# Performance work log

Measured on AMD Instinct MI355X. Metric: run time of the kernel, lower is better.

The kernel has to match this reference:

```python
import jax, jax.numpy as jnp
import numpy as np

N_ITEMS = 1_000_000
IN_DIM, HID_DIM, OUT_DIM = 64, 256, 128
N_BINS = 4096


def setup_inputs() -> dict:
    key = jax.random.key(0)
    k1, k2, k3, k4 = jax.random.split(key, 4)
    x = jax.random.normal(k1, (N_ITEMS, IN_DIM), dtype=jnp.float32)
    idxs = jax.random.randint(k2, (N_ITEMS,), 0, N_BINS, dtype=jnp.int64)
    W1 = jax.random.normal(k3, (IN_DIM, HID_DIM), dtype=jnp.float32) * (1.0 / np.sqrt(IN_DIM))
    b1 = jnp.zeros((HID_DIM,), dtype=jnp.float32)
    W2 = jax.random.normal(k4, (HID_DIM, OUT_DIM), dtype=jnp.float32) * (1.0 / np.sqrt(HID_DIM))
    b2 = jnp.zeros((OUT_DIM,), dtype=jnp.float32)
    return {"x": x, "idxs": idxs, "n_bins": N_BINS, "W1": W1, "b1": b1, "W2": W2, "b2": b2}


def reference(x, idxs, n_bins, W1, b1, W2, b2):
    # MLP: Linear -> ReLU -> Linear (per item)
    h = jax.nn.relu(x @ W1 + b1)            # [N, HID]
    items_encoded = h @ W2 + b2             # [N, OUT]
    # scatter-add into bins (torch.index_put_ with accumulate=True)
    embeddings = jax.ops.segment_sum(items_encoded, idxs, num_segments=n_bins)  # [n_bins, OUT]
    return embeddings
```

## Files before the change

### kernel.cpp

```cpp
#include <hip/hip_runtime.h>
#include <hip/hip_bf16.h>

typedef __attribute__((ext_vector_type(8))) short short8;
typedef __attribute__((ext_vector_type(4))) float f32x4;
typedef __attribute__((ext_vector_type(4))) int int4v;

#define CAPB  384
#define NSCAT 64
#define NBINS 4096

__device__ inline unsigned short f2bf(float f) {
  unsigned u = __float_as_uint(f);
  return (unsigned short)((u + 0x7FFFu + ((u >> 16) & 1u)) >> 16);
}
__device__ inline short bfc(float f) {
  __hip_bfloat16 h = __float2bfloat16(f);
  return *(short*)&h;
}
__device__ inline __attribute__((always_inline))
f32x4 mfma16(short8 a, short8 b, f32x4 c) {
  return __builtin_amdgcn_mfma_f32_16x16x32_bf16(a, b, c, 0, 0, 0);
}
__device__ __forceinline__ void gload_lds16(const void* g, void* l) {
  __builtin_amdgcn_global_load_lds(
      (const __attribute__((address_space(1))) void*)g,
      (__attribute__((address_space(3))) void*)l, 16, 0, 0);
}

__global__ __launch_bounds__(256)
void bin_hist(const int* __restrict__ idxs, int* __restrict__ wsCnt,
              int* __restrict__ wsOff, int n_items)
{
  __shared__ int hist[NBINS];
  const int tid = threadIdx.x;
  for (int b = tid; b < NBINS; b += 256) hist[b] = 0;
  __syncthreads();

  const int nq = n_items >> 2;
  const int chunk = (nq + NSCAT - 1) / NSCAT;
  const int s0 = blockIdx.x * chunk;
  const int s1 = min(nq, s0 + chunk);
  const int4v* idx4 = (const int4v*)idxs;
  for (int s = s0 + tid; s < s1; s += 256) {
    int4v v = idx4[s];
    atomicAdd(&hist[v[0]], 1);
    atomicAdd(&hist[v[1]], 1);
    atomicAdd(&hist[v[2]], 1);
    atomicAdd(&hist[v[3]], 1);
  }
  if (blockIdx.x == NSCAT - 1)
    for (int i = (nq << 2) + tid; i < n_items; i += 256)
      atomicAdd(&hist[idxs[i]], 1);
  __syncthreads();

  for (int b = tid; b < NBINS; b += 256) {
    int c = hist[b];
    if (c) wsOff[b * NSCAT + blockIdx.x] = atomicAdd(&wsCnt[b], c);
  }
}

__global__ __launch_bounds__(256)
void scatter_ids(const int* __restrict__ idxs, const int* __restrict__ wsOff,
                 int* __restrict__ wsIds, int n_items)
{
  __shared__ int cur[NBINS];
  const int tid = threadIdx.x;
  for (int b = tid; b < NBINS; b += 256) cur[b] = wsOff[b * NSCAT + blockIdx.x];
  __syncthreads();

  const int nq = n_items >> 2;
  const int chunk = (nq + NSCAT - 1) / NSCAT;
  const int s0 = blockIdx.x * chunk;
  const int s1 = min(nq, s0 + chunk);
  const int4v* idx4 = (const int4v*)idxs;
  for (int s = s0 + tid; s < s1; s += 256) {
    int4v v = idx4[s];
    #pragma unroll
    for (int e = 0; e < 4; ++e) {
      int b = v[e];
      int pos = atomicAdd(&cur[b], 1);
      if (pos < CAPB) wsIds[b * CAPB + pos] = s * 4 + e;
    }
  }
  if (blockIdx.x == NSCAT - 1)
    for (int i = (nq << 2) + tid; i < n_items; i += 256) {
      int b = idxs[i];
      int pos = atomicAdd(&cur[b], 1);
      if (pos < CAPB) wsIds[b * CAPB + pos] = i;
    }
}

#define LDS_BYTES 153344

__global__ __launch_bounds__(512)
void mlp_bin8(const float* __restrict__ x,
              const float* __restrict__ W1,
              const float* __restrict__ b1,
              const float* __restrict__ W2,
              const float* __restrict__ b2,
              const int* __restrict__ wsCnt,
              const int* __restrict__ wsIds,
              float* __restrict__ out)
{
  extern __shared__ char smem[];
  unsigned short* sW1 = (unsigned short*)smem;
  char*           sStage = smem + 32768;
  unsigned short* sW2 = (unsigned short*)(smem + 32768);
  float* sB1 = (float*)(smem + 131072);
  float* sB2 = (float*)(smem + 132096);
  unsigned short* sHs = (unsigned short*)(smem + 132608);
  int*   sIds = (int*)(smem + 141056);

  const int tid = threadIdx.x;
  const int myblk = blockIdx.x;

  for (int f = tid; f < 16384; f += 512) {
    int blk = f >> 9;
    int mt = blk >> 1, kt = blk & 1;
    int ln = (f >> 3) & 63, j = f & 7;
    int qq = ln >> 4, cc = ln & 15;
    sW1[f] = f2bf(W1[(32*kt + 8*qq + j)*256 + 16*mt + cc]);
  }
  if (tid < 256) sB1[tid] = b1[tid];
  if (tid < 128) sB2[tid] = b2[tid];
  __syncthreads();

  const int lane = tid & 63;
  const int wave = tid >> 6;
  const int c = lane & 15;
  const int q = lane >> 4;
  char* myStage = sStage + wave * 12288;
  int*  myIds   = sIds + wave * 384;

  auto issue = [&](int pp, int bb, int cnt) {
    char* dst = myStage + bb * 4096;
    #pragma unroll
    for (int i = 0; i < 4; ++i) {
      int r = i*4 + (lane >> 4);
      int slot = pp*16 + r;
      int id = myIds[min(slot, cnt - 1)];
      int g = (lane & 15) ^ (r & 7);
      gload_lds16(x + (long)id * 64 + g * 4, dst + i * 1024);
    }
  };

  #pragma unroll 1
  for (int bsel = 0; bsel < 2; ++bsel) {
    const int lb = wave * 2 + bsel;
    const int gbin = myblk * 16 + lb;
    const int cnt = min(wsCnt[gbin], CAPB);
    const int passes = (cnt + 15) >> 4;
    const int* idsG = wsIds + gbin * CAPB;

    for (int j = lane; j < cnt; j += 64) myIds[j] = idsG[j];
    asm volatile("s_waitcnt vmcnt(0)" ::: "memory");

    float hsum[8][8];
    #pragma unroll
    for (int a = 0; a < 8; ++a)
      #pragma unroll
      for (int bq = 0; bq < 8; ++bq) hsum[a][bq] = 0.f;

    if (passes > 0) issue(0, 0, cnt);
    if (passes > 1) issue(1, 1, cnt);

    int bi = 0;
    for (int p = 0; p < passes; ++p) {
      if (p + 2 < passes) {
        int nb = bi + 2; if (nb >= 3) nb -= 3;
        issue(p + 2, nb, cnt);
        asm volatile("s_waitcnt vmcnt(8)" ::: "memory");
      } else if (p + 1 < passes) {
        asm volatile("s_waitcnt vmcnt(4)" ::: "memory");
      } else {
        asm volatile("s_waitcnt vmcnt(0)" ::: "memory");
      }
      const char* buf = myStage + bi * 4096;
      if (++bi >= 3) bi = 0;

      f32x4 v00 = *(const f32x4*)(buf + c*256 + (((2*q + 0)) ^ (c & 7))*16);
      f32x4 v01 = *(const f32x4*)(buf + c*256 + (((2*q + 1)) ^ (c & 7))*16);
      f32x4 v10 = *(const f32x4*)(buf + c*256 + (((8 + 2*q + 0)) ^ (c & 7))*16);
      f32x4 v11 = *(const f32x4*)(buf + c*256 + (((8 + 2*q + 1)) ^ (c & 7))*16);
      short8 xf0, xf1;
      xf0[0]=bfc(v00[0]); xf0[1]=bfc(v00[1]); xf0[2]=bfc(v00[2]); xf0[3]=bfc(v00[3]);
      xf0[4]=bfc(v01[0]); xf0[5]=bfc(v01[1]); xf0[6]=bfc(v01[2]); xf0[7]=bfc(v01[3]);
      xf1[0]=bfc(v10[0]); xf1[1]=bfc(v10[1]); xf1[2]=bfc(v10[2]); xf1[3]=bfc(v10[3]);
      xf1[4]=bfc(v11[0]); xf1[5]=bfc(v11[1]); xf1[6]=bfc(v11[2]); xf1[7]=bfc(v11[3]);
      const bool valid = (p*16 + c) < cnt;
      short8 z = {0,0,0,0,0,0,0,0};
      xf0 = valid ? xf0 : z;
      xf1 = valid ? xf1 : z;

      #pragma unroll
      for (int kt2 = 0; kt2 < 8; ++kt2) {
        #pragma unroll
        for (int half = 0; half < 2; ++half) {
          const int mt = 2*kt2 + half;
          f32x4 g1 = *(const f32x4*)(sB1 + 16*mt + 4*q);
          short8 w0 = *(const short8*)(sW1 + (mt*2 + 0)*512 + lane*8);
          g1 = mfma16(w0, xf0, g1);
          short8 w1 = *(const short8*)(sW1 + (mt*2 + 1)*512 + lane*8);
          g1 = mfma16(w1, xf1, g1);
          #pragma unroll
          for (int r = 0; r < 4; ++r)
            hsum[kt2][half*4 + r] += fmaxf(g1[r], 0.f);
        }
      }
    }

    const int n_inv = passes*16 - cnt;
    if (n_inv > 0) {
      const float fn = (float)n_inv;
      #pragma unroll
      for (int kt2 = 0; kt2 < 8; ++kt2)
        #pragma unroll
        for (int half = 0; half < 2; ++half)
          #pragma unroll
          for (int r = 0; r < 4; ++r)
            hsum[kt2][half*4 + r] -= fn * fmaxf(sB1[16*(2*kt2+half) + 4*q + r], 0.f);
    }

    #pragma unroll
    for (int a = 0; a < 8; ++a)
      #pragma unroll
      for (int bq = 0; bq < 8; ++bq) {
        float v = hsum[a][bq];
        v += __shfl_xor(v, 1);
        v += __shfl_xor(v, 2);
        v += __shfl_xor(v, 4);
        v += __shfl_xor(v, 8);
        hsum[a][bq] = v;
      }

    if (c == 0) {
      #pragma unroll
      for (int kt2 = 0; kt2 < 8; ++kt2)
        #pragma unroll
        for (int half = 0; half < 2; ++half) {
          unsigned d0 = (unsigned)f2bf(hsum[kt2][half*4+0]) | ((unsigned)f2bf(hsum[kt2][half*4+1]) << 16);
          unsigned d1 = (unsigned)f2bf(hsum[kt2][half*4+2]) | ((unsigned)f2bf(hsum[kt2][half*4+3]) << 16);
          unsigned* dst = (unsigned*)(sHs + lb*264 + kt2*32 + half*16 + 4*q);
          dst[0] = d0; dst[1] = d1;
        }
    }
  }
  __syncthreads();

  for (int f = tid; f < 32768; f += 512) {
    int blk = f >> 9;
    int mt2 = blk >> 3, kt2 = blk & 7;
    int ln = (f >> 3) & 63, j = f & 7;
    int qq = ln >> 4, cc = ln & 15;
    sW2[f] = f2bf(W2[(32*kt2 + 8*qq + j)*128 + 16*mt2 + cc]);
  }
  __syncthreads();

  {
    const int mt2 = wave;
    f32x4 acc = {0.f, 0.f, 0.f, 0.f};
    #pragma unroll
    for (int kt2 = 0; kt2 < 8; ++kt2) {
      short8 w2 = *(const short8*)(sW2 + (mt2*8 + kt2)*512 + lane*8);
      short8 hf = *(const short8*)(sHs + c*264 + kt2*32 + 8*q);
      acc = mfma16(w2, hf, acc);
    }
    const int cntc = min(wsCnt[myblk*16 + c], CAPB);
    f32x4 res;
    #pragma unroll
    for (int r = 0; r < 4; ++r)
      res[r] = acc[r] + (float)cntc * sB2[16*mt2 + 4*q + r];
    float* op = out + ((long)myblk*16 + c)*128 + 16*mt2 + 4*q;
    *(f32x4*)op = res;
  }
}

extern "C" void kernel_launch(void* const* d_in, const int* in_sizes, int n_in,
                              void* d_out, int out_size, void* d_ws, size_t ws_size,
                              hipStream_t stream) {
  const float* x  = (const float*)d_in[0];
  const int* idxs = (const int*)d_in[1];
  const float* W1 = (const float*)d_in[3];
  const float* b1 = (const float*)d_in[4];
  const float* W2 = (const float*)d_in[5];
  const float* b2 = (const float*)d_in[6];
  float* out = (float*)d_out;
  const int n_items = in_sizes[1];
  const int n_bins = out_size / 128;
  const int nblocks = n_bins / 16;

  int* wsCnt = (int*)d_ws;
  int* wsOff = wsCnt + NBINS;
  int* wsIds = wsOff + NBINS * NSCAT;

  hipMemsetAsync(wsCnt, 0, (size_t)n_bins * sizeof(int), stream);
  bin_hist<<<NSCAT, 256, 0, stream>>>(idxs, wsCnt, wsOff, n_items);
  scatter_ids<<<NSCAT, 256, 0, stream>>>(idxs, wsOff, wsIds, n_items);
  mlp_bin8<<<nblocks, 512, LDS_BYTES, stream>>>(x, W1, b1, W2, b2, wsCnt, wsIds, out);
}
```

Baseline: 135.1 us.

## Process two staged row-tiles per iteration and double scatter grid size

The main loop now handles passes in pairs. Each iteration converts two 16-row tiles, then issues the next two prefetches into a 3-buffer ring, and interleaves independent MFMA chains for both tiles. This gives more independent MFMA work and longer latency hiding between global loads. Pass count is rounded up to even, so padded rows get extra work, corrected through the invalid-row bias subtraction. NSCAT doubles to 128 blocks for the histogram and scatter kernels, spreading the binning work over more workgroups.

```diff
diff --git a/kernel.cpp b/kernel.cpp
--- a/kernel.cpp
+++ b/kernel.cpp
@@ -6,7 +6,7 @@
 typedef __attribute__((ext_vector_type(4))) int int4v;
 
 #define CAPB  384
-#define NSCAT 64
+#define NSCAT 128
 #define NBINS 4096
 
 __device__ inline unsigned short f2bf(float f) {
@@ -93,7 +93,7 @@
 #define LDS_BYTES 153344
 
 __global__ __launch_bounds__(512)
-void mlp_bin8(const float* __restrict__ x,
+void mlp_bin9(const float* __restrict__ x,
               const float* __restrict__ W1,
               const float* __restrict__ b1,
               const float* __restrict__ W2,
@@ -132,8 +132,8 @@
   char* myStage = sStage + wave * 12288;
   int*  myIds   = sIds + wave * 384;
 
-  auto issue = [&](int pp, int bb, int cnt) {
-    char* dst = myStage + bb * 4096;
+  auto issue = [&](int pp, int cnt) {
+    char* dst = myStage + (pp % 3) * 4096;
     #pragma unroll
     for (int i = 0; i < 4; ++i) {
       int r = i*4 + (lane >> 4);
@@ -143,6 +143,20 @@
       gload_lds16(x + (long)id * 64 + g * 4, dst + i * 1024);
     }
   };
+  auto cvtrow = [&](const char* buf, bool valid, short8& o0, short8& o1) {
+    f32x4 v00 = *(const f32x4*)(buf + c*256 + (((2*q + 0)) ^ (c & 7))*16);
+    f32x4 v01 = *(const f32x4*)(buf + c*256 + (((2*q + 1)) ^ (c & 7))*16);
+    f32x4 v10 = *(const f32x4*)(buf + c*256 + (((8 + 2*q + 0)) ^ (c & 7))*16);
+    f32x4 v11 = *(const f32x4*)(buf + c*256 + (((8 + 2*q + 1)) ^ (c & 7))*16);
+    short8 f0, f1;
+    f0[0]=bfc(v00[0]); f0[1]=bfc(v00[1]); f0[2]=bfc(v00[2]); f0[3]=bfc(v00[3]);
+    f0[4]=bfc(v01[0]); f0[5]=bfc(v01[1]); f0[6]=bfc(v01[2]); f0[7]=bfc(v01[3]);
+    f1[0]=bfc(v10[0]); f1[1]=bfc(v10[1]); f1[2]=bfc(v10[2]); f1[3]=bfc(v10[3]);
+    f1[4]=bfc(v11[0]); f1[5]=bfc(v11[1]); f1[6]=bfc(v11[2]); f1[7]=bfc(v11[3]);
+    short8 z = {0,0,0,0,0,0,0,0};
+    o0 = valid ? f0 : z;
+    o1 = valid ? f1 : z;
+  };
 
   #pragma unroll 1
   for (int bsel = 0; bsel < 2; ++bsel) {
@@ -150,6 +164,7 @@
     const int gbin = myblk * 16 + lb;
     const int cnt = min(wsCnt[gbin], CAPB);
     const int passes = (cnt + 15) >> 4;
+    const int npass2 = ((passes + 1) >> 1) << 1;
     const int* idsG = wsIds + gbin * CAPB;
 
     for (int j = lane; j < cnt; j += 64) myIds[j] = idsG[j];
@@ -161,55 +176,49 @@
       #pragma unroll
       for (int bq = 0; bq < 8; ++bq) hsum[a][bq] = 0.f;
 
-    if (passes > 0) issue(0, 0, cnt);
-    if (passes > 1) issue(1, 1, cnt);
-
-    int bi = 0;
-    for (int p = 0; p < passes; ++p) {
-      if (p + 2 < passes) {
-        int nb = bi + 2; if (nb >= 3) nb -= 3;
-        issue(p + 2, nb, cnt);
-        asm volatile("s_waitcnt vmcnt(8)" ::: "memory");
-      } else if (p + 1 < passes) {
+    if (npass2 > 0) {
+      issue(0, cnt);
+      issue(1, cnt);
+      if (2 < npass2) issue(2, cnt);
+    }
+
+    for (int pp = 0; pp < npass2; pp += 2) {
+      if (pp + 2 < npass2) {
         asm volatile("s_waitcnt vmcnt(4)" ::: "memory");
       } else {
         asm volatile("s_waitcnt vmcnt(0)" ::: "memory");
       }
-      const char* buf = myStage + bi * 4096;
-      if (++bi >= 3) bi = 0;
-
-      f32x4 v00 = *(const f32x4*)(buf + c*256 + (((2*q + 0)) ^ (c & 7))*16);
-      f32x4 v01 = *(const f32x4*)(buf + c*256 + (((2*q + 1)) ^ (c & 7))*16);
-      f32x4 v10 = *(const f32x4*)(buf + c*256 + (((8 + 2*q + 0)) ^ (c & 7))*16);
-      f32x4 v11 = *(const f32x4*)(buf + c*256 + (((8 + 2*q + 1)) ^ (c & 7))*16);
-      short8 xf0, xf1;
-      xf0[0]=bfc(v00[0]); xf0[1]=bfc(v00[1]); xf0[2]=bfc(v00[2]); xf0[3]=bfc(v00[3]);
-      xf0[4]=bfc(v01[0]); xf0[5]=bfc(v01[1]); xf0[6]=bfc(v01[2]); xf0[7]=bfc(v01[3]);
-      xf1[0]=bfc(v10[0]); xf1[1]=bfc(v10[1]); xf1[2]=bfc(v10[2]); xf1[3]=bfc(v10[3]);
-      xf1[4]=bfc(v11[0]); xf1[5]=bfc(v11[1]); xf1[6]=bfc(v11[2]); xf1[7]=bfc(v11[3]);
-      const bool valid = (p*16 + c) < cnt;
-      short8 z = {0,0,0,0,0,0,0,0};
-      xf0 = valid ? xf0 : z;
-      xf1 = valid ? xf1 : z;
+      const char* bufA = myStage + ((pp    ) % 3) * 4096;
+      const char* bufB = myStage + ((pp + 1) % 3) * 4096;
+
+      short8 xfA[2], xfB[2];
+      cvtrow(bufA, (pp*16 + c) < cnt, xfA[0], xfA[1]);
+      cvtrow(bufB, ((pp+1)*16 + c) < cnt, xfB[0], xfB[1]);
+
+      if (pp + 3 < npass2) issue(pp + 3, cnt);
+      if (pp + 4 < npass2) issue(pp + 4, cnt);
 
       #pragma unroll
       for (int kt2 = 0; kt2 < 8; ++kt2) {
         #pragma unroll
         for (int half = 0; half < 2; ++half) {
           const int mt = 2*kt2 + half;
-          f32x4 g1 = *(const f32x4*)(sB1 + 16*mt + 4*q);
+          f32x4 bias = *(const f32x4*)(sB1 + 16*mt + 4*q);
+          f32x4 gA = bias, gB = bias;
           short8 w0 = *(const short8*)(sW1 + (mt*2 + 0)*512 + lane*8);
-          g1 = mfma16(w0, xf0, g1);
+          gA = mfma16(w0, xfA[0], gA);
+          gB = mfma16(w0, xfB[0], gB);
           short8 w1 = *(const short8*)(sW1 + (mt*2 + 1)*512 + lane*8);
-          g1 = mfma16(w1, xf1, g1);
+          gA = mfma16(w1, xfA[1], gA);
+          gB = mfma16(w1, xfB[1], gB);
           #pragma unroll
           for (int r = 0; r < 4; ++r)
-            hsum[kt2][half*4 + r] += fmaxf(g1[r], 0.f);
+            hsum[kt2][half*4 + r] += fmaxf(gA[r], 0.f) + fmaxf(gB[r], 0.f);
         }
       }
     }
 
-    const int n_inv = passes*16 - cnt;
+    const int n_inv = npass2*16 - cnt;
     if (n_inv > 0) {
       const float fn = (float)n_inv;
       #pragma unroll
@@ -296,5 +305,5 @@
   hipMemsetAsync(wsCnt, 0, (size_t)n_bins * sizeof(int), stream);
   bin_hist<<<NSCAT, 256, 0, stream>>>(idxs, wsCnt, wsOff, n_items);
   scatter_ids<<<NSCAT, 256, 0, stream>>>(idxs, wsOff, wsIds, n_items);
-  mlp_bin8<<<nblocks, 512, LDS_BYTES, stream>>>(x, W1, b1, W2, b2, wsCnt, wsIds, out);
-}
+  mlp_bin9<<<nblocks, 512, LDS_BYTES, stream>>>(x, W1, b1, W2, b2, wsCnt, wsIds, out);
+}
```

New measurement: 123.7 us. 1.09x faster.
